# Kernel optimization log

Measured on AMD Instinct MI355X. Metric: run time of the kernel, lower is better.

The kernel has to match this reference:

```python
import jax, jax.numpy as jnp
from jax import lax
import numpy as np

N, T, V = 32, 32, 128
C_FEAT, C_BOX, C_CLS = 256, 4, 4
C_IN = C_FEAT + C_BOX + C_CLS  # 264 (is_scene=False concatenates x,b,c)
C_OUT = 64
K = 9
EPS = 1e-3  # keras BatchNormalization default epsilon


def _bn4(x, g, b, m, v):
    # inference-mode BN over channel axis 1 of (N,C,T,V)
    s = (g * lax.rsqrt(v + EPS))[None, :, None, None]
    return (x - m[None, :, None, None]) * s + b[None, :, None, None]


def _stgcn(x, a, imp, w, bw, ga, ba, ma, va, al, wt, bt, gb, bb, mb, vb, residual):
    res = x if residual else 0.0
    # SGCN: 1x1 conv (channels_first) then adjacency aggregation; dropout is identity at inference
    h = jnp.einsum('nctv,co->notv', x, w) + bw[None, :, None, None]
    h = jnp.einsum('nctv,ntvw->nctw', h, a * imp)
    # TGCN: BN -> PReLU(alpha per (C,T,V)) -> temporal conv (K,1) SAME -> BN -> (dropout=id)
    h = _bn4(h, ga, ba, ma, va)
    h = jnp.where(h >= 0, h, al[None] * h)
    h = lax.conv_general_dilated(h, wt, (1, 1), 'SAME',
                                 dimension_numbers=('NCHW', 'HWIO', 'NCHW')) + bt[None, :, None, None]
    h = _bn4(h, gb, bb, mb, vb)
    return h + res  # use_mdn=True -> no final PReLU


def _forward(x, b, c, a, dbn_g, dbn_b, dbn_m, dbn_v,
             w0, bw0, imp0, g0a, b0a, m0a, v0a, al0, wt0, bt0, g0b, b0b, m0b, v0b,
             w1, bw1, imp1, g1a, b1a, m1a, v1a, al1, wt1, bt1, g1b, b1b, m1b, v1b):
    x = jnp.concatenate([x, b, c], axis=-1)  # (N,T,V,C_IN)
    n, t, v, cc = x.shape
    # data BN over flattened (V*C) channel axis, exactly as the TF reshapes do
    x = jnp.transpose(x, (0, 2, 3, 1)).reshape(n, v * cc, t)
    s = (dbn_g * lax.rsqrt(dbn_v + EPS))[None, :, None]
    x = (x - dbn_m[None, :, None]) * s + dbn_b[None, :, None]
    # NOTE: the original does transpose(0,1,3,2) then a *reshape* to (N,C,T,V); replicate exactly
    x = x.reshape(n, v, cc, t).transpose(0, 1, 3, 2).reshape(n, cc, t, v)
    x = _stgcn(x, a, imp0, w0, bw0, g0a, b0a, m0a, v0a, al0, wt0, bt0, g0b, b0b, m0b, v0b, residual=False)
    x = _stgcn(x, a, imp1, w1, bw1, g1a, b1a, m1a, v1a, al1, wt1, bt1, g1b, b1b, m1b, v1b, residual=True)
    x = x[:, :, :, 0]  # (N,C_OUT,T)
    return jnp.transpose(x, (0, 2, 1))  # (N,T,C_OUT)


def setup_inputs():
    key = jax.random.key(0)
    ks = jax.random.split(key, 40)
    rn = lambda k, s, sc=1.0: jax.random.normal(k, s, jnp.float32) * sc
    ru = lambda k, s, lo, hi: jax.random.uniform(k, s, jnp.float32, lo, hi)
    d = {}
    d['x'] = rn(ks[0], (N, T, V, C_FEAT))
    d['b'] = rn(ks[1], (N, T, V, C_BOX))
    d['c'] = ru(ks[2], (N, T, V, C_CLS), 0.0, 1.0)
    d['a'] = ru(ks[3], (N, T, V, V), 0.0, 1.0)
    d['dbn_g'] = ru(ks[4], (V * C_IN,), 0.5, 1.5)
    d['dbn_b'] = rn(ks[5], (V * C_IN,), 0.1)
    d['dbn_m'] = rn(ks[6], (V * C_IN,), 0.1)
    d['dbn_v'] = ru(ks[7], (V * C_IN,), 0.5, 1.5)

    def mk_layer(i, cin, kb):
        d['w%d' % i] = rn(ks[kb], (cin, C_OUT), (1.0 / cin) ** 0.5)
        d['bw%d' % i] = rn(ks[kb + 1], (C_OUT,), 0.01)
        d['imp%d' % i] = rn(ks[kb + 2], (V, V), (2.0 / (V * V)) ** 0.5)
        d['g%da' % i] = ru(ks[kb + 3], (C_OUT,), 0.5, 1.5)
        d['b%da' % i] = rn(ks[kb + 4], (C_OUT,), 0.1)
        d['m%da' % i] = rn(ks[kb + 5], (C_OUT,), 0.1)
        d['v%da' % i] = ru(ks[kb + 6], (C_OUT,), 0.5, 1.5)
        d['al%d' % i] = ru(ks[kb + 7], (C_OUT, T, V), 0.0, 0.3)
        d['wt%d' % i] = rn(ks[kb + 8], (K, 1, C_OUT, C_OUT), (1.0 / (K * C_OUT)) ** 0.5)
        d['bt%d' % i] = rn(ks[kb + 9], (C_OUT,), 0.01)
        d['g%db' % i] = ru(ks[kb + 10], (C_OUT,), 0.5, 1.5)
        d['b%db' % i] = rn(ks[kb + 11], (C_OUT,), 0.1)
        d['m%db' % i] = rn(ks[kb + 12], (C_OUT,), 0.1)
        d['v%db' % i] = ru(ks[kb + 13], (C_OUT,), 0.5, 1.5)

    mk_layer(0, C_IN, 8)
    mk_layer(1, C_OUT, 22)
    return d


def reference(x, b, c, a, dbn_g, dbn_b, dbn_m, dbn_v,
              w0, bw0, imp0, g0a, b0a, m0a, v0a, al0, wt0, bt0, g0b, b0b, m0b, v0b,
              w1, bw1, imp1, g1a, b1a, m1a, v1a, al1, wt1, bt1, g1b, b1b, m1b, v1b):
    return _forward(x, b, c, a, dbn_g, dbn_b, dbn_m, dbn_v,
                    w0, bw0, imp0, g0a, b0a, m0a, v0a, al0, wt0, bt0, g0b, b0b, m0b, v0b,
                    w1, bw1, imp1, g1a, b1a, m1a, v1a, al1, wt1, bt1, g1b, b1b, m1b, v1b)
```

## Files before the change

kernel.cpp:

```cpp
#include <hip/hip_runtime.h>
#include <hip/hip_bf16.h>

typedef unsigned short u16;
typedef unsigned int   u32;

#define N_   32
#define T_   32
#define V_   128
#define CIN_ 264
#define CO_  64
#define KT_  9
#define EPS_ 1e-3f

#define OFF_DBN_S 0
#define OFF_DBN_O 33792
#define OFF_W0    67584
#define OFF_BW0   84480
#define OFF_A0S   84544
#define OFF_A0O   84608
#define OFF_B0S   84672
#define OFF_B0O   84736
#define OFF_W1    84800
#define OFF_BW1   88896
#define OFF_A1S   88960
#define OFF_A1O   89024
#define OFF_B1S   89088
#define OFF_B1O   89152
#define PREP_TOTAL 110464

#define B_P    0
#define B_FLAG 360448
#define B_W0A  360512
#define B_WTA  397440
#define B_H0   524288
#define B_G0   (B_H0 + 16777216)
#define B_L0   (B_G0 + 16777216)
#define B_G1P  (B_L0 + 33554432)
#define B_END  (B_G1P + 262144)

typedef short bf16x8 __attribute__((ext_vector_type(8)));
typedef float f32x4  __attribute__((ext_vector_type(4)));

__device__ __forceinline__ float bf2f(u16 u) { return __uint_as_float(((u32)u) << 16); }
__device__ __forceinline__ u16 f2bf(float f) {
    u32 x = __float_as_uint(f);
    return (u16)((x + 0x7fffu + ((x >> 16) & 1u)) >> 16);
}
__device__ __forceinline__ float ldin(const void* p, u32 i, int f32) {
    return f32 ? ((const float*)p)[i] : bf2f(((const u16*)p)[i]);
}

__global__ void k_detect(const void* a, int* flag) {
    if (threadIdx.x == 0 && blockIdx.x == 0) {
        const u16* p = (const u16*)a;
        int cnt = 0;
        for (int i = 0; i < 64; ++i) {
            float v = bf2f(p[2 * i]);
            if (v >= 0.f && v <= 1.0f) ++cnt;
        }
        *flag = (cnt >= 56) ? 0 : 1;
    }
}

__global__ void k_prep(const void* dbn_g, const void* dbn_b, const void* dbn_m, const void* dbn_v,
                       const void* w0, const void* bw0,
                       const void* g0a, const void* b0a, const void* m0a, const void* v0a,
                       const void* bt0, const void* g0b, const void* b0b, const void* m0b, const void* v0b,
                       const void* w1, const void* bw1,
                       const void* g1a, const void* b1a, const void* m1a, const void* v1a,
                       const void* bt1, const void* g1b, const void* b1b, const void* m1b, const void* v1b,
                       const void* wt0,
                       float* P, u16* W0A, u16* WTA, const int* flagp)
{
    const int f32 = *flagp;
    int i = blockIdx.x * 256 + threadIdx.x;
    if (i < 33792) {
        float s = ldin(dbn_g, i, f32) * rsqrtf(ldin(dbn_v, i, f32) + EPS_);
        P[OFF_DBN_S + i] = s;
        P[OFF_DBN_O + i] = ldin(dbn_b, i, f32) - ldin(dbn_m, i, f32) * s;
    } else if (i < 50688) { int j = i - 33792; P[OFF_W0 + j] = ldin(w0, j, f32); }
    else if (i < 50752) { int j = i - 50688; P[OFF_BW0 + j] = ldin(bw0, j, f32); }
    else if (i < 50816) { int j = i - 50752;
        float s = ldin(g0a, j, f32) * rsqrtf(ldin(v0a, j, f32) + EPS_);
        P[OFF_A0S + j] = s; P[OFF_A0O + j] = ldin(b0a, j, f32) - ldin(m0a, j, f32) * s;
    } else if (i < 50880) { int j = i - 50816;
        float s = ldin(g0b, j, f32) * rsqrtf(ldin(v0b, j, f32) + EPS_);
        P[OFF_B0S + j] = s; P[OFF_B0O + j] = (ldin(bt0, j, f32) - ldin(m0b, j, f32)) * s + ldin(b0b, j, f32);
    } else if (i < 54976) { int j = i - 50880; P[OFF_W1 + j] = ldin(w1, j, f32); }
    else if (i < 55040) { int j = i - 54976; P[OFF_BW1 + j] = ldin(bw1, j, f32); }
    else if (i < 55104) { int j = i - 55040;
        float s = ldin(g1a, j, f32) * rsqrtf(ldin(v1a, j, f32) + EPS_);
        P[OFF_A1S + j] = s; P[OFF_A1O + j] = ldin(b1a, j, f32) - ldin(m1a, j, f32) * s;
    } else if (i < 55168) { int j = i - 55104;
        float s = ldin(g1b, j, f32) * rsqrtf(ldin(v1b, j, f32) + EPS_);
        P[OFF_B1S + j] = s; P[OFF_B1O + j] = (ldin(bt1, j, f32) - ldin(m1b, j, f32)) * s + ldin(b1b, j, f32);
    } else if (i < 73600) {
        int j = i - 55168; int c = j / 288, ci = j - c * 288;
        float val = (ci < 264) ? ldin(w0, (u32)ci * 64 + c, f32)
                  : ((ci == 264) ? ldin(bw0, c, f32) : 0.f);
        W0A[j] = f2bf(val);
    } else if (i < 110464) {
        int j = i - 73600; int k = j >> 12, rem = j & 4095, o = rem >> 6, ii = rem & 63;
        WTA[j] = f2bf(ldin(wt0, ((u32)(k * 64 + ii)) * 64 + o, f32));
    }
}

__global__ __launch_bounds__(256) void k_pw0(const void* __restrict__ xin, const void* __restrict__ bin,
                                             const void* __restrict__ cin2, const float* __restrict__ P,
                                             const u16* __restrict__ W0Ag, u16* __restrict__ h0,
                                             const int* __restrict__ flagp)
{
    __shared__ __align__(16) u16 XT[64 * 296];
    const int f32 = *flagp;
    const int t2 = blockIdx.x, n = blockIdx.y, vh = blockIdx.z;
    const int tid = threadIdx.x;
    const int vbase = vh * 64;
    for (int e = tid; e < 288 * 64; e += 256) {
        int c2 = e >> 6, vloc = e & 63;
        int vv = vbase + vloc;
        float val;
        if (c2 < 264) {
            u32 L = (u32)c2 * 4096u + (u32)t2 * 128u + (u32)vv;
            u32 vs = L / 8448u;
            u32 r  = L - vs * 8448u;
            u32 ts = r / 264u;
            u32 cc = r - ts * 264u;
            u32 base = ((u32)n * 32u + ts) * 128u + vs;
            if (cc < 256u)      val = ldin(xin, base * 256u + cc, f32);
            else if (cc < 260u) val = ldin(bin, base * 4u + (cc - 256u), f32);
            else                val = ldin(cin2, base * 4u + (cc - 260u), f32);
            u32 ch = vs * 264u + cc;
            val = fmaf(val, P[OFF_DBN_S + ch], P[OFF_DBN_O + ch]);
        } else val = (c2 == 264) ? 1.0f : 0.0f;
        XT[vloc * 296 + c2] = f2bf(val);
    }
    __syncthreads();
    const int wv = tid >> 6, lane = tid & 63, l16 = lane & 15, quad = lane >> 4;
    const int m0 = wv * 16;
    f32x4 acc[4];
#pragma unroll
    for (int i = 0; i < 4; ++i) acc[i] = (f32x4){0.f, 0.f, 0.f, 0.f};
    for (int ks = 0; ks < 9; ++ks) {
        const int k0 = ks * 32 + quad * 8;
        bf16x8 af = *(const bf16x8*)&XT[(m0 + l16) * 296 + k0];
#pragma unroll
        for (int ni = 0; ni < 4; ++ni) {
            bf16x8 bf = *(const bf16x8*)&W0Ag[(u32)(ni * 16 + l16) * 288 + k0];
            acc[ni] = __builtin_amdgcn_mfma_f32_16x16x32_bf16(af, bf, acc[ni], 0, 0, 0);
        }
    }
    const int v = vbase + m0 + quad * 4;
#pragma unroll
    for (int ni = 0; ni < 4; ++ni) {
        int c = ni * 16 + l16;
        ushort4 rr; u16* rp = (u16*)&rr;
#pragma unroll
        for (int r = 0; r < 4; ++r) rp[r] = f2bf(acc[ni][r]);
        *(ushort4*)&h0[((u32)(n * 64 + c) * 32 + t2) * 128 + v] = rr;
    }
}

__global__ __launch_bounds__(256) void k_graph0(const void* __restrict__ a, const void* __restrict__ imp0,
                                                const void* __restrict__ al0, const float* __restrict__ P,
                                                const u16* __restrict__ h0, u16* __restrict__ g0,
                                                const int* __restrict__ flagp)
{
    __shared__ __align__(16) u16 amT[128 * 136];
    __shared__ __align__(16) u16 Hs[64 * 136];
    const int f32 = *flagp;
    const int t = blockIdx.x, n = blockIdx.y;
    const int tid = threadIdx.x;
    const u32 abase = (((u32)n * T_ + t) * V_) * V_;
    for (int e = tid; e < 128 * 128; e += 256) {
        int vv = e >> 7, w = e & 127;
        float av = ldin(a, abase + (u32)vv * 128u + w, f32) * ldin(imp0, (u32)vv * 128u + w, f32);
        amT[w * 136 + vv] = f2bf(av);
    }
    for (int e = tid; e < 1024; e += 256) {
        int c = e >> 4, ch = e & 15;
        *(uint4*)&Hs[c * 136 + ch * 8] = *(const uint4*)&h0[((u32)(n * 64 + c) * 32 + t) * 128 + ch * 8];
    }
    __syncthreads();
    const int wv = tid >> 6, lane = tid & 63, l16 = lane & 15, quad = lane >> 4;
    const int n0w = wv * 32;
    f32x4 acc[4][2];
#pragma unroll
    for (int mi = 0; mi < 4; ++mi) { acc[mi][0] = (f32x4){0,0,0,0}; acc[mi][1] = (f32x4){0,0,0,0}; }
#pragma unroll
    for (int ks = 0; ks < 4; ++ks) {
        const int k0 = ks * 32 + quad * 8;
        bf16x8 bf[2];
        bf[0] = *(const bf16x8*)&amT[(n0w + l16) * 136 + k0];
        bf[1] = *(const bf16x8*)&amT[(n0w + 16 + l16) * 136 + k0];
#pragma unroll
        for (int mi = 0; mi < 4; ++mi) {
            bf16x8 af = *(const bf16x8*)&Hs[(mi * 16 + l16) * 136 + k0];
            acc[mi][0] = __builtin_amdgcn_mfma_f32_16x16x32_bf16(af, bf[0], acc[mi][0], 0, 0, 0);
            acc[mi][1] = __builtin_amdgcn_mfma_f32_16x16x32_bf16(af, bf[1], acc[mi][1], 0, 0, 0);
        }
    }
#pragma unroll
    for (int mi = 0; mi < 4; ++mi) {
        const int c0 = mi * 16 + quad * 4;
        const float4 s4 = *(const float4*)&P[OFF_A0S + c0];
        const float4 o4 = *(const float4*)&P[OFF_A0O + c0];
        const float ss[4] = {s4.x, s4.y, s4.z, s4.w};
        const float oo[4] = {o4.x, o4.y, o4.z, o4.w};
#pragma unroll
        for (int ni = 0; ni < 2; ++ni) {
            const int w = n0w + ni * 16 + l16;
            ushort4 rr; u16* rp = (u16*)&rr;
#pragma unroll
            for (int r = 0; r < 4; ++r) {
                float y = fmaf(acc[mi][ni][r], ss[r], oo[r]);
                float alv = ldin(al0, ((u32)(c0 + r) * 32 + t) * 128 + w, f32);
                rp[r] = f2bf((y >= 0.f) ? y : alv * y);
            }
            *(ushort4*)&g0[((u32)(n * 32 + t) * 128 + w) * 64 + c0] = rr;
        }
    }
}

__global__ __launch_bounds__(256) void k_tconv0(const u16* __restrict__ WTAg, const float* __restrict__ P,
                                                const u16* __restrict__ g0, float* __restrict__ L0)
{
    __shared__ __align__(16) u16 Wl[2][64 * 72];
    __shared__ __align__(16) u16 Bs[2][128 * 72];
    const int t = blockIdx.x, n = blockIdx.y;
    const int tid = threadIdx.x;
    const int kmin = (t < 4) ? (4 - t) : 0;
    const int kmax = (t > 27) ? (35 - t) : 8;

    auto stageB = [&](int k, int buf) {
        const u16* src = g0 + ((u32)(n * 32 + (t + k - 4)) * 128) * 64;
        for (int e = tid; e < 1024; e += 256) {
            int row = e >> 3, ch = e & 7;
            *(uint4*)&Bs[buf][row * 72 + ch * 8] = *(const uint4*)&src[row * 64 + ch * 8];
        }
    };
    auto stageW = [&](int k, int buf) {
        const u16* src = WTAg + (u32)k * 4096;
        for (int e = tid; e < 512; e += 256) {
            int row = e >> 3, ch = e & 7;
            *(uint4*)&Wl[buf][row * 72 + ch * 8] = *(const uint4*)&src[row * 64 + ch * 8];
        }
    };
    stageB(kmin, 0); stageW(kmin, 0);
    __syncthreads();
    const int wv = tid >> 6, lane = tid & 63, l16 = lane & 15, quad = lane >> 4;
    const int n0w = wv * 32;
    f32x4 acc[4][2];
#pragma unroll
    for (int mi = 0; mi < 4; ++mi) { acc[mi][0] = (f32x4){0,0,0,0}; acc[mi][1] = (f32x4){0,0,0,0}; }

    for (int k = kmin; k <= kmax; ++k) {
        const int buf = (k - kmin) & 1;
        if (k < kmax) { stageB(k + 1, buf ^ 1); stageW(k + 1, buf ^ 1); }
#pragma unroll
        for (int ks = 0; ks < 2; ++ks) {
            const int k0 = ks * 32 + quad * 8;
            bf16x8 bf[2];
            bf[0] = *(const bf16x8*)&Bs[buf][(n0w + l16) * 72 + k0];
            bf[1] = *(const bf16x8*)&Bs[buf][(n0w + 16 + l16) * 72 + k0];
#pragma unroll
            for (int mi = 0; mi < 4; ++mi) {
                bf16x8 af = *(const bf16x8*)&Wl[buf][(mi * 16 + l16) * 72 + k0];
                acc[mi][0] = __builtin_amdgcn_mfma_f32_16x16x32_bf16(af, bf[0], acc[mi][0], 0, 0, 0);
                acc[mi][1] = __builtin_amdgcn_mfma_f32_16x16x32_bf16(af, bf[1], acc[mi][1], 0, 0, 0);
            }
        }
        __syncthreads();
    }
#pragma unroll
    for (int mi = 0; mi < 4; ++mi) {
        const int ob = mi * 16 + quad * 4;
        const float4 s4 = *(const float4*)&P[OFF_B0S + ob];
        const float4 o4 = *(const float4*)&P[OFF_B0O + ob];
        const float ss[4] = {s4.x, s4.y, s4.z, s4.w};
        const float oo[4] = {o4.x, o4.y, o4.z, o4.w};
#pragma unroll
        for (int ni = 0; ni < 2; ++ni) {
            const int v = n0w + ni * 16 + l16;
#pragma unroll
            for (int r = 0; r < 4; ++r)
                L0[((u32)(n * 64 + ob + r) * 32 + t) * 128 + v] = fmaf(acc[mi][ni][r], ss[r], oo[r]);
        }
    }
}

__global__ __launch_bounds__(128) void k_pw1(const void* __restrict__ a, const void* __restrict__ imp1,
                                             const void* __restrict__ al1, const float* __restrict__ P,
                                             const float* __restrict__ L0, float* __restrict__ g1p,
                                             const int* __restrict__ flagp)
{
    __shared__ float part[V_ * 65];
    __shared__ float red2[128];
    const int f32 = *flagp;
    const int t = blockIdx.x, n = blockIdx.y;
    const int tid = threadIdx.x;
    const int v = tid;
    float acc[CO_];
#pragma unroll
    for (int o = 0; o < CO_; ++o) acc[o] = P[OFF_BW1 + o];
    const float* W = P + OFF_W1;
    const u32 base = (u32)n * (CO_ * T_ * V_) + (u32)t * V_ + (u32)v;
    for (int c = 0; c < CO_; ++c) {
        float xv = L0[base + (u32)c * (T_ * V_)];
        const float* wr = W + c * CO_;
#pragma unroll
        for (int o = 0; o < CO_; ++o) acc[o] = fmaf(xv, wr[o], acc[o]);
    }
    float amv = ldin(a, (((u32)n * T_ + t) * V_ + v) * V_ + 0u, f32) * ldin(imp1, (u32)v * V_ + 0u, f32);
#pragma unroll
    for (int o = 0; o < CO_; ++o) part[v * 65 + o] = acc[o] * amv;
    __syncthreads();
    const int o = tid & 63, hh = tid >> 6;
    float s = 0.f;
    for (int vv = hh * 64; vv < hh * 64 + 64; ++vv) s += part[vv * 65 + o];
    red2[tid] = s;
    __syncthreads();
    if (tid < 64) {
        float g = red2[tid] + red2[64 + tid];
        float y = fmaf(g, P[OFF_A1S + o], P[OFF_A1O + o]);
        float alv = ldin(al1, ((u32)o * T_ + t) * V_ + 0u, f32);
        y = (y >= 0.f) ? y : alv * y;
        g1p[((u32)n * CO_ + o) * T_ + t] = y;
    }
}

__global__ __launch_bounds__(64) void k_tconv1(const void* __restrict__ wt1, const float* __restrict__ P,
                                               const float* __restrict__ g1p, const float* __restrict__ L0,
                                               void* __restrict__ out, const int* __restrict__ flagp)
{
    __shared__ float gl[CO_ * KT_];
    const int f32 = *flagp;
    const int t = blockIdx.x, n = blockIdx.y;
    const int tid = threadIdx.x;
    for (int e = tid; e < CO_ * KT_; e += 64) {
        int i = e / KT_, kk = e - i * KT_;
        int tt = t + kk - 4;
        gl[e] = (tt >= 0 && tt < T_) ? g1p[((u32)n * CO_ + i) * T_ + tt] : 0.f;
    }
    __syncthreads();
    float acc = 0.f;
    for (int i = 0; i < CO_; ++i) {
#pragma unroll
        for (int k = 0; k < KT_; ++k) {
            float wv = ldin(wt1, ((u32)(k * CO_ + i)) * CO_ + tid, f32);
            acc = fmaf(gl[i * KT_ + k], wv, acc);
        }
    }
    float y = fmaf(acc, P[OFF_B1S + tid], P[OFF_B1O + tid]);
    y += L0[(u32)n * (CO_ * T_ * V_) + (u32)tid * (T_ * V_) + (u32)t * V_ + 0];
    const u32 oi = ((u32)n * T_ + t) * CO_ + tid;
    if (f32) ((float*)out)[oi] = y;
    else     ((u16*)out)[oi]   = f2bf(y);
}

__global__ void k_fail(u16* out, int nel) {
    int i = blockIdx.x * 256 + threadIdx.x;
    if (i < nel) out[i] = 0x7f80;
}

extern "C" void kernel_launch(void* const* d_in, const int* in_sizes, int n_in,
                              void* d_out, int out_size, void* d_ws, size_t ws_size,
                              hipStream_t stream)
{
    const void* xin  = d_in[0];
    const void* bin  = d_in[1];
    const void* cin2 = d_in[2];
    const void* a    = d_in[3];
    const void* dbn_g = d_in[4];
    const void* dbn_b = d_in[5];
    const void* dbn_m = d_in[6];
    const void* dbn_v = d_in[7];
    const void* w0  = d_in[8];
    const void* bw0 = d_in[9];
    const void* imp0 = d_in[10];
    const void* g0a = d_in[11];
    const void* b0a = d_in[12];
    const void* m0a = d_in[13];
    const void* v0a = d_in[14];
    const void* al0 = d_in[15];
    const void* wt0 = d_in[16];
    const void* bt0 = d_in[17];
    const void* g0b = d_in[18];
    const void* b0b = d_in[19];
    const void* m0b = d_in[20];
    const void* v0b = d_in[21];
    const void* w1  = d_in[22];
    const void* bw1 = d_in[23];
    const void* imp1 = d_in[24];
    const void* g1a = d_in[25];
    const void* b1a = d_in[26];
    const void* m1a = d_in[27];
    const void* v1a = d_in[28];
    const void* al1 = d_in[29];
    const void* wt1 = d_in[30];
    const void* bt1 = d_in[31];
    const void* g1b = d_in[32];
    const void* b1b = d_in[33];
    const void* m1b = d_in[34];
    const void* v1b = d_in[35];

    if (ws_size < (size_t)B_END) {
        k_fail<<<(out_size + 255) / 256, 256, 0, stream>>>((u16*)d_out, out_size);
        return;
    }
    char* w = (char*)d_ws;
    float* P    = (float*)(w + B_P);
    int*   flg  = (int*)(w + B_FLAG);
    u16*   W0A  = (u16*)(w + B_W0A);
    u16*   WTA  = (u16*)(w + B_WTA);
    u16*   h0   = (u16*)(w + B_H0);
    u16*   g0   = (u16*)(w + B_G0);
    float* L0   = (float*)(w + B_L0);
    float* g1p  = (float*)(w + B_G1P);

    k_detect<<<1, 64, 0, stream>>>(a, flg);
    k_prep<<<(PREP_TOTAL + 255) / 256, 256, 0, stream>>>(
        dbn_g, dbn_b, dbn_m, dbn_v, w0, bw0, g0a, b0a, m0a, v0a,
        bt0, g0b, b0b, m0b, v0b, w1, bw1, g1a, b1a, m1a, v1a,
        bt1, g1b, b1b, m1b, v1b, wt0, P, W0A, WTA, flg);

    dim3 gpw0(T_, N_, 2);
    dim3 grid(T_, N_);
    k_pw0   <<<gpw0, 256, 0, stream>>>(xin, bin, cin2, P, W0A, h0, flg);
    k_graph0<<<grid, 256, 0, stream>>>(a, imp0, al0, P, h0, g0, flg);
    k_tconv0<<<grid, 256, 0, stream>>>(WTA, P, g0, L0);
    k_pw1   <<<grid, 128, 0, stream>>>(a, imp1, al1, P, L0, g1p, flg);
    k_tconv1<<<grid,  64, 0, stream>>>(wt1, P, g1p, L0, d_out, flg);
}
```

Measured before the change: 594.6 us.

## Split input BN/transpose into coalesced staging kernel before pointwise GEMM

Moves the data-BN, concatenate and reshape gather out of k_pw0 into a new k_bnx kernel. k_bnx reads the inputs with 4-wide vector loads, transposes them through shared memory and writes a bf16 row-major staging buffer. k_pw0 then feeds MFMA A-fragments directly from that buffer and injects the bias column in-register. This replaces scalar, divide-heavy gathers with vector loads. The cost is an extra global round-trip of the staged activations, processed in two batch halves that reuse the later g0/L0 workspace.

```diff
diff --git a/kernel.cpp b/kernel.cpp
--- a/kernel.cpp
+++ b/kernel.cpp
@@ -33,6 +33,7 @@
 #define B_W0A  360512
 #define B_WTA  397440
 #define B_H0   524288
+#define B_XP   (B_H0 + 16777216)
 #define B_G0   (B_H0 + 16777216)
 #define B_L0   (B_G0 + 16777216)
 #define B_G1P  (B_L0 + 33554432)
@@ -105,51 +106,101 @@
     }
 }
 
-__global__ __launch_bounds__(256) void k_pw0(const void* __restrict__ xin, const void* __restrict__ bin,
+__global__ __launch_bounds__(256) void k_bnx(const void* __restrict__ xin, const void* __restrict__ bin,
                                              const void* __restrict__ cin2, const float* __restrict__ P,
-                                             const u16* __restrict__ W0Ag, u16* __restrict__ h0,
-                                             const int* __restrict__ flagp)
-{
-    __shared__ __align__(16) u16 XT[64 * 296];
+                                             u16* __restrict__ Xp, const int* __restrict__ flagp, int nbase)
+{
+    __shared__ __align__(16) u16 tile[32 * 130];
     const int f32 = *flagp;
-    const int t2 = blockIdx.x, n = blockIdx.y, vh = blockIdx.z;
-    const int tid = threadIdx.x;
-    const int vbase = vh * 64;
-    for (int e = tid; e < 288 * 64; e += 256) {
-        int c2 = e >> 6, vloc = e & 63;
-        int vv = vbase + vloc;
-        float val;
-        if (c2 < 264) {
-            u32 L = (u32)c2 * 4096u + (u32)t2 * 128u + (u32)vv;
-            u32 vs = L / 8448u;
-            u32 r  = L - vs * 8448u;
-            u32 ts = r / 264u;
-            u32 cc = r - ts * 264u;
-            u32 base = ((u32)n * 32u + ts) * 128u + vs;
-            if (cc < 256u)      val = ldin(xin, base * 256u + cc, f32);
-            else if (cc < 260u) val = ldin(bin, base * 4u + (cc - 256u), f32);
-            else                val = ldin(cin2, base * 4u + (cc - 260u), f32);
-            u32 ch = vs * 264u + cc;
-            val = fmaf(val, P[OFF_DBN_S + ch], P[OFF_DBN_O + ch]);
-        } else val = (c2 == 264) ? 1.0f : 0.0f;
-        XT[vloc * 296 + c2] = f2bf(val);
-    }
-    __syncthreads();
+    const int rt = blockIdx.x;
+    const int ct = blockIdx.y;
+    const int nloc = blockIdx.z;
+    const int n = nbase + nloc;
+    const int c0 = ct * 32;
+    const int ncols = (ct == 8) ? 8 : 32;
+    const int r0 = rt * 128;
+    const int tid = threadIdx.x;
+
+    for (int q = tid; q < ncols * 32; q += 256) {
+        int j = q >> 5, i4 = (q & 31) << 2;
+        u32 L = (u32)(c0 + j) * 4096u + (u32)(r0 + i4);
+        u32 vs = L / 8448u;
+        u32 r  = L - vs * 8448u;
+        u32 ts = r / 264u;
+        u32 cc = r - ts * 264u;
+        u32 base = ((u32)n * 32u + ts) * 128u + vs;
+        float4 val;
+        if (f32) {
+            if (cc < 256u)      val = *(const float4*)((const float*)xin  + (size_t)base * 256u + cc);
+            else if (cc < 260u) val = *(const float4*)((const float*)bin  + (size_t)base * 4u + (cc - 256u));
+            else                val = *(const float4*)((const float*)cin2 + (size_t)base * 4u + (cc - 260u));
+        } else {
+            ushort4 uv;
+            if (cc < 256u)      uv = *(const ushort4*)((const u16*)xin  + (size_t)base * 256u + cc);
+            else if (cc < 260u) uv = *(const ushort4*)((const u16*)bin  + (size_t)base * 4u + (cc - 256u));
+            else                uv = *(const ushort4*)((const u16*)cin2 + (size_t)base * 4u + (cc - 260u));
+            val.x = bf2f(uv.x); val.y = bf2f(uv.y); val.z = bf2f(uv.z); val.w = bf2f(uv.w);
+        }
+        u32 ch = vs * 264u + cc;
+        const float4 s4 = *(const float4*)&P[OFF_DBN_S + ch];
+        const float4 o4 = *(const float4*)&P[OFF_DBN_O + ch];
+        ushort2 lo, hi;
+        lo.x = f2bf(fmaf(val.x, s4.x, o4.x));
+        lo.y = f2bf(fmaf(val.y, s4.y, o4.y));
+        hi.x = f2bf(fmaf(val.z, s4.z, o4.z));
+        hi.y = f2bf(fmaf(val.w, s4.w, o4.w));
+        *(ushort2*)&tile[j * 130 + i4]     = lo;
+        *(ushort2*)&tile[j * 130 + i4 + 2] = hi;
+    }
+    __syncthreads();
+    const int chunks = ncols >> 3;
+    for (int e = tid; e < 128 * chunks; e += 256) {
+        int i, cch;
+        if (chunks == 4) { i = e >> 2; cch = e & 3; } else { i = e; cch = 0; }
+        __align__(16) u16 tmp[8];
+#pragma unroll
+        for (int k2 = 0; k2 < 8; ++k2) tmp[k2] = tile[(cch * 8 + k2) * 130 + i];
+        *(uint4*)&Xp[((u32)nloc * 4096u + (u32)(r0 + i)) * 264u + (u32)(c0 + cch * 8)] = *(uint4*)tmp;
+    }
+}
+
+__global__ __launch_bounds__(256) void k_pw0(const u16* __restrict__ Xp, const u16* __restrict__ W0Ag,
+                                             u16* __restrict__ h0, int nbase)
+{
+    const int t2 = blockIdx.x, nloc = blockIdx.y, vh = blockIdx.z;
+    const int n = nbase + nloc;
+    const int tid = threadIdx.x;
     const int wv = tid >> 6, lane = tid & 63, l16 = lane & 15, quad = lane >> 4;
     const int m0 = wv * 16;
+    const int vrow = vh * 64 + m0 + l16;
+    const u16* arow = Xp + ((u32)nloc * 4096u + (u32)(t2 * 128 + vrow)) * 264u;
+
     f32x4 acc[4];
 #pragma unroll
     for (int i = 0; i < 4; ++i) acc[i] = (f32x4){0.f, 0.f, 0.f, 0.f};
-    for (int ks = 0; ks < 9; ++ks) {
+
+#pragma unroll
+    for (int ks = 0; ks < 8; ++ks) {
         const int k0 = ks * 32 + quad * 8;
-        bf16x8 af = *(const bf16x8*)&XT[(m0 + l16) * 296 + k0];
+        bf16x8 af = *(const bf16x8*)&arow[k0];
 #pragma unroll
         for (int ni = 0; ni < 4; ++ni) {
             bf16x8 bf = *(const bf16x8*)&W0Ag[(u32)(ni * 16 + l16) * 288 + k0];
             acc[ni] = __builtin_amdgcn_mfma_f32_16x16x32_bf16(af, bf, acc[ni], 0, 0, 0);
         }
     }
-    const int v = vbase + m0 + quad * 4;
+    {
+        bf16x8 af = (bf16x8){0, 0, 0, 0, 0, 0, 0, 0};
+        if (quad == 0)      af = *(const bf16x8*)&arow[256];
+        else if (quad == 1) af[0] = (short)0x3F80;
+        const int k0 = 256 + quad * 8;
+#pragma unroll
+        for (int ni = 0; ni < 4; ++ni) {
+            bf16x8 bf = *(const bf16x8*)&W0Ag[(u32)(ni * 16 + l16) * 288 + k0];
+            acc[ni] = __builtin_amdgcn_mfma_f32_16x16x32_bf16(af, bf, acc[ni], 0, 0, 0);
+        }
+    }
+    const int v = vh * 64 + m0 + quad * 4;
 #pragma unroll
     for (int ni = 0; ni < 4; ++ni) {
         int c = ni * 16 + l16;
@@ -413,6 +464,7 @@
     u16*   W0A  = (u16*)(w + B_W0A);
     u16*   WTA  = (u16*)(w + B_WTA);
     u16*   h0   = (u16*)(w + B_H0);
+    u16*   Xp   = (u16*)(w + B_XP);
     u16*   g0   = (u16*)(w + B_G0);
     float* L0   = (float*)(w + B_L0);
     float* g1p  = (float*)(w + B_G1P);
@@ -423,9 +475,13 @@
         bt0, g0b, b0b, m0b, v0b, w1, bw1, g1a, b1a, m1a, v1a,
         bt1, g1b, b1b, m1b, v1b, wt0, P, W0A, WTA, flg);
 
-    dim3 gpw0(T_, N_, 2);
+    for (int hf = 0; hf < 2; ++hf) {
+        const int nbase = hf * 16;
+        k_bnx<<<dim3(32, 9, 16), 256, 0, stream>>>(xin, bin, cin2, P, Xp, flg, nbase);
+        k_pw0<<<dim3(T_, 16, 2), 256, 0, stream>>>(Xp, W0A, h0, nbase);
+    }
+
     dim3 grid(T_, N_);
-    k_pw0   <<<gpw0, 256, 0, stream>>>(xin, bin, cin2, P, W0A, h0, flg);
     k_graph0<<<grid, 256, 0, stream>>>(a, imp0, al0, P, h0, g0, flg);
     k_tconv0<<<grid, 256, 0, stream>>>(WTA, P, g0, L0);
     k_pw1   <<<grid, 128, 0, stream>>>(a, imp1, al1, P, L0, g1p, flg);
```

Result: faster. 561.3 us (-5.6%).
